# Performance work log

Measured on AMD Instinct MI355X. Metric: run time of the kernel, lower is better.

The kernel has to match this reference:

```python
import jax, jax.numpy as jnp
import numpy as np

N_NODES = 100000

def gcn_conv(x, edge_index, W, b, n_nodes):
    # GCNConv: out = D^{-1/2} (A + I) D^{-1/2} X W + b  (self-loops added)
    src, dst = edge_index[0], edge_index[1]
    loops = jnp.arange(n_nodes, dtype=edge_index.dtype)
    src = jnp.concatenate([src, loops])
    dst = jnp.concatenate([dst, loops])
    deg = jax.ops.segment_sum(jnp.ones_like(dst, dtype=x.dtype), dst, num_segments=n_nodes)
    dinv = jnp.where(deg > 0, jax.lax.rsqrt(deg), 0.0)
    norm = dinv[src] * dinv[dst]  # [E+N]
    h = x @ W  # transform first (small d), then gather/scatter
    msgs = h[src] * norm[:, None]
    out = jax.ops.segment_sum(msgs, dst, num_segments=n_nodes)
    return out + b


def setup_inputs() -> dict:
    key = jax.random.key(0)
    k1, k2, k3, k4, k5, k6 = jax.random.split(key, 6)
    x = jax.random.normal(k1, (N_NODES, 3), dtype=jnp.float32)
    edge_index = jax.random.randint(k2, (2, 2400000), 0, N_NODES, dtype=jnp.int64)
    # Glorot-style init for GCNConv linear weights; zero bias matches PyG default
    W1 = jax.random.normal(k3, (3, 16), dtype=jnp.float32) * (1.0 / np.sqrt(3))
    b1 = jnp.zeros((16,), dtype=jnp.float32)
    W2 = jax.random.normal(k4, (16, 32), dtype=jnp.float32) * (1.0 / np.sqrt(16))
    b2 = jnp.zeros((32,), dtype=jnp.float32)
    return {"x": x, "edge_index": edge_index, "W1": W1, "b1": b1, "W2": W2, "b2": b2}


def reference(x, edge_index, W1, b1, W2, b2):
    n = x.shape[0]
    h = gcn_conv(x, edge_index, W1, b1, n)
    h = jax.nn.relu(h)
    h = gcn_conv(h, edge_index, W2, b2, n)
    # batch is all zeros in the original forward -> single-graph mean pool
    return jnp.mean(h, axis=0, keepdims=True)  # [1, 32]
```

## Files before the change

### kernel.cpp

```cpp
#include <hip/hip_runtime.h>

typedef unsigned int uint;
typedef unsigned long long ull;


#define MAXB  256
#define CAP   16384u
#define BINB  512
#define CHUNK 4096
#define SPL   8
#define PADN  131072
#define AFS   2048.0f
#define AFB   16384
#define AFM   0x1FFFFFu

__device__ __forceinline__ uint slice_lo(uint c, uint s) {
    return (s == 0u) ? 0u : ((c * s / SPL) & ~7u);
}
__device__ __forceinline__ uint slice_hi(uint c, uint s) {
    return (s == SPL - 1u) ? c : ((c * (s + 1u) / SPL) & ~7u);
}

__global__ void __launch_bounds__(BINB)
bin_kernel(const int* __restrict__ key, const int* __restrict__ other,
           uint* __restrict__ cursor, uint* __restrict__ buf, int E) {
    __shared__ uint cnt[MAXB], scanb[MAXB], baseb[MAXB];
    __shared__ uint stage[CHUNK];
    const int tid = threadIdx.x;
    const int e0 = blockIdx.x * CHUNK;
    const int nE = min(CHUNK, E - e0);
    const int my0 = tid * 8;
    const int myc = max(0, min(8, nE - my0));
    if (tid < MAXB) cnt[tid] = 0u;

    uint k8[8], o8[8], r8[8];
    if (myc == 8) {
        int4 ka = ((const int4*)(key + e0))[tid * 2];
        int4 kb = ((const int4*)(key + e0))[tid * 2 + 1];
        int4 oa = ((const int4*)(other + e0))[tid * 2];
        int4 ob = ((const int4*)(other + e0))[tid * 2 + 1];
        k8[0] = ka.x; k8[1] = ka.y; k8[2] = ka.z; k8[3] = ka.w;
        k8[4] = kb.x; k8[5] = kb.y; k8[6] = kb.z; k8[7] = kb.w;
        o8[0] = oa.x; o8[1] = oa.y; o8[2] = oa.z; o8[3] = oa.w;
        o8[4] = ob.x; o8[5] = ob.y; o8[6] = ob.z; o8[7] = ob.w;
    } else {
        for (int r = 0; r < myc; ++r) {
            k8[r] = (uint)key[e0 + my0 + r];
            o8[r] = (uint)other[e0 + my0 + r];
        }
    }
    __syncthreads();
    for (int r = 0; r < myc; ++r) r8[r] = atomicAdd(&cnt[k8[r] >> 9], 1u);
    __syncthreads();
    if (tid < MAXB) scanb[tid] = cnt[tid];
    __syncthreads();
    for (int d = 1; d < MAXB; d <<= 1) {
        uint t = (tid < MAXB && tid >= d) ? scanb[tid - d] : 0u;
        __syncthreads();
        if (tid < MAXB) scanb[tid] += t;
        __syncthreads();
    }
    if (tid < MAXB) baseb[tid] = (uint)tid * CAP + (cnt[tid] ? atomicAdd(&cursor[tid * 16], cnt[tid]) : 0u);
    __syncthreads();
    for (int r = 0; r < myc; ++r) {
        uint b = k8[r] >> 9;
        stage[(scanb[b] - cnt[b]) + r8[r]] = ((k8[r] & 511u) << 17) | o8[r];
    }
    __syncthreads();
    const int wave = tid >> 6, lane = tid & 63;
    for (int b = wave; b < MAXB; b += BINB / 64) {
        uint s0 = scanb[b] - cnt[b], c = cnt[b], gb = baseb[b];
        uint lim = (uint)(b + 1) * CAP;
        for (uint i = lane; i < c; i += 64u) {
            uint gp = gb + i;
            if (gp < lim) buf[gp] = stage[s0 + i];
        }
    }
}

__global__ void __launch_bounds__(256)
deg_kernel(const uint* __restrict__ buf, const uint* __restrict__ curD,
           uint* __restrict__ degg, int n) {
    __shared__ uint dg[512];
    const int tid = threadIdx.x;
    const int b = blockIdx.x >> 3;
    const uint s = blockIdx.x & 7;
    const uint base = (uint)b * CAP;
    const uint c = min(curD[b * 16], CAP);
    const uint lo = slice_lo(c, s), hi = slice_hi(c, s);
    dg[tid] = 0u; dg[tid + 256] = 0u;
    __syncthreads();
    for (uint i0 = lo + (uint)tid * 8u; i0 < hi; i0 += 2048u) {
        uint cnt8 = min(8u, hi - i0);
        uint en[8];
        if (cnt8 == 8u) {
            uint4 a = ((const uint4*)(buf + base + i0))[0];
            uint4 bb = ((const uint4*)(buf + base + i0))[1];
            en[0] = a.x; en[1] = a.y; en[2] = a.z; en[3] = a.w;
            en[4] = bb.x; en[5] = bb.y; en[6] = bb.z; en[7] = bb.w;
        } else {
            for (uint r = 0; r < cnt8; ++r) en[r] = buf[base + i0 + r];
        }
        for (uint r = 0; r < cnt8; ++r) atomicAdd(&dg[en[r] >> 17], 1u);
    }
    __syncthreads();
    for (int t = tid; t < 512; t += 256) {
        int node = (b << 9) + t;
        if (node < n && dg[t]) atomicAdd(&degg[node], dg[t]);
    }
}

__global__ void node1_kernel(const float* __restrict__ x, const uint* __restrict__ degg,
                             float* __restrict__ dinv, float4* __restrict__ xd4, int n) {
    int i = blockIdx.x * blockDim.x + threadIdx.x;
    if (i >= n) return;
    float di = rsqrtf((float)(degg[i] + 1u));
    dinv[i] = di;
    xd4[i] = make_float4(x[3 * i] * di, x[3 * i + 1] * di, x[3 * i + 2] * di, di);
}

__global__ void __launch_bounds__(256)
agg_kernel(const uint* __restrict__ buf, const uint* __restrict__ curD,
           const float4* __restrict__ xd4, ull* __restrict__ accp, int n) {
    __shared__ ull acc[512];
    const int tid = threadIdx.x;
    const int b = blockIdx.x >> 3;
    const uint s = blockIdx.x & 7;
    const uint base = (uint)b * CAP;
    const uint c = min(curD[b * 16], CAP);
    const uint lo = slice_lo(c, s), hi = slice_hi(c, s);
    acc[tid] = 0ull; acc[tid + 256] = 0ull;
    __syncthreads();
    for (uint i0 = lo + (uint)tid * 8u; i0 < hi + 8u * 2048u; i0 += 2048u) {
        if (i0 >= hi) continue;
        uint cnt8 = min(8u, hi - i0);
        uint en[8];
        if (cnt8 == 8u) {
            uint4 a = ((const uint4*)(buf + base + i0))[0];
            uint4 bb = ((const uint4*)(buf + base + i0))[1];
            en[0] = a.x; en[1] = a.y; en[2] = a.z; en[3] = a.w;
            en[4] = bb.x; en[5] = bb.y; en[6] = bb.z; en[7] = bb.w;
        } else {
            for (uint r = 0; r < cnt8; ++r) en[r] = buf[base + i0 + r];
            for (uint r = cnt8; r < 8u; ++r) en[r] = en[0];
        }
        float4 gv[8];
#pragma unroll
        for (int r = 0; r < 8; ++r) gv[r] = xd4[en[r] & 0x1FFFFu];
#pragma unroll
        for (uint r = 0; r < 8u; ++r) {
            if (r < cnt8) {
                uint dl = en[r] >> 17;
                ull f0 = (ull)(uint)((int)rintf(gv[r].x * AFS) + AFB);
                ull f1 = (ull)(uint)((int)rintf(gv[r].y * AFS) + AFB);
                ull f2 = (ull)(uint)((int)rintf(gv[r].z * AFS) + AFB);
                atomicAdd(&acc[dl], f0 | (f1 << 21) | (f2 << 42));
            }
        }
    }
    __syncthreads();
    for (int t = tid; t < 512; t += 256) {
        ull v = acc[t];
        int node = (b << 9) + t;
        if (v && node < n) atomicAdd(&accp[node], v);
    }
}

__global__ void __launch_bounds__(256)
q_kernel(const ull* __restrict__ accp, const uint* __restrict__ degg,
         const float4* __restrict__ xd4, const float* __restrict__ W1,
         const float* __restrict__ b1, uint4* __restrict__ qb,
         float* __restrict__ T, int n) {
    __shared__ float tacc[16];
    const int tid = threadIdx.x;
    if (tid < 16) tacc[tid] = 0.0f;
    __syncthreads();
    int i = blockIdx.x * blockDim.x + tid;
    float sq[16];
    if (i < n) {
        float4 sv = xd4[i];
        float di = sv.w;
        ull v = accp[i];
        int ub = (int)(degg[i] * (uint)AFB);
        const float isc = 1.0f / AFS;
        float a = (float)((int)(uint)(v & AFM) - ub) * isc + sv.x;
        float b = (float)((int)(uint)((v >> 21) & AFM) - ub) * isc + sv.y;
        float c = (float)((int)(uint)((v >> 42) & AFM) - ub) * isc + sv.z;
        float q[16];
#pragma unroll
        for (int k = 0; k < 16; ++k) {
            float h = di * (a * W1[k] + b * W1[16 + k] + c * W1[32 + k]) + b1[k];
            h = fmaxf(h, 0.0f);
            q[k] = di * h;
            sq[k] = di * q[k];
        }
        uint pk[8];
#pragma unroll
        for (int k = 0; k < 8; ++k) {
            uint l = __float_as_uint(q[2 * k]);
            l = (l + 0x7FFFu + ((l >> 16) & 1u)) >> 16;
            uint h2 = __float_as_uint(q[2 * k + 1]);
            h2 = ((h2 + 0x7FFFu + ((h2 >> 16) & 1u)) & 0xFFFF0000u);
            pk[k] = l | h2;
        }
        qb[2 * (size_t)i]     = make_uint4(pk[0], pk[1], pk[2], pk[3]);
        qb[2 * (size_t)i + 1] = make_uint4(pk[4], pk[5], pk[6], pk[7]);
    } else {
#pragma unroll
        for (int k = 0; k < 16; ++k) sq[k] = 0.0f;
    }
#pragma unroll
    for (int k = 0; k < 16; ++k) {
        float v = sq[k];
        for (int off = 32; off > 0; off >>= 1) v += __shfl_down(v, off, 64);
        if ((tid & 63) == 0) atomicAdd(&tacc[k], v);
    }
    __syncthreads();
    if (tid < 16) atomicAdd(&T[tid], tacc[tid]);
}

__global__ void __launch_bounds__(256)
T_kernel(const uint* __restrict__ buf, const uint* __restrict__ curD,
         const float* __restrict__ dinv, const uint4* __restrict__ qb,
         float* __restrict__ T, int n) {
    __shared__ float dt[512];
    __shared__ float tacc[16];
    const int tid = threadIdx.x;
    const int b = blockIdx.x >> 3;
    const uint s = blockIdx.x & 7;
    const uint base = (uint)b * CAP;
    const uint c = min(curD[b * 16], CAP);
    const uint lo = slice_lo(c, s), hi = slice_hi(c, s);
    for (int t = tid; t < 512; t += 256) {
        int node = (b << 9) + t;
        dt[t] = (node < n) ? dinv[node] : 0.0f;
    }
    if (tid < 16) tacc[tid] = 0.0f;
    __syncthreads();
    float rac[16];
#pragma unroll
    for (int k = 0; k < 16; ++k) rac[k] = 0.0f;
    for (uint i0 = lo + (uint)tid * 8u; i0 < hi + 8u * 2048u; i0 += 2048u) {
        if (i0 >= hi) continue;
        uint cnt8 = min(8u, hi - i0);
        uint en[8];
        if (cnt8 == 8u) {
            uint4 a = ((const uint4*)(buf + base + i0))[0];
            uint4 bb = ((const uint4*)(buf + base + i0))[1];
            en[0] = a.x; en[1] = a.y; en[2] = a.z; en[3] = a.w;
            en[4] = bb.x; en[5] = bb.y; en[6] = bb.z; en[7] = bb.w;
        } else {
            for (uint r = 0; r < cnt8; ++r) en[r] = buf[base + i0 + r];
            for (uint r = cnt8; r < 8u; ++r) en[r] = en[0];
        }
        uint4 qa[8], qc[8];
#pragma unroll
        for (int r = 0; r < 8; ++r) {
            uint sv = en[r] & 0x1FFFFu;
            qa[r] = qb[2 * (size_t)sv];
            qc[r] = qb[2 * (size_t)sv + 1];
        }
#pragma unroll
        for (uint r = 0; r < 8u; ++r) {
            if (r < cnt8) {
                float di = dt[en[r] >> 17];
                uint w[8] = {qa[r].x, qa[r].y, qa[r].z, qa[r].w,
                             qc[r].x, qc[r].y, qc[r].z, qc[r].w};
#pragma unroll
                for (int k = 0; k < 8; ++k) {
                    rac[2 * k]     += di * __uint_as_float(w[k] << 16);
                    rac[2 * k + 1] += di * __uint_as_float(w[k] & 0xFFFF0000u);
                }
            }
        }
    }
#pragma unroll
    for (int k = 0; k < 16; ++k) {
        float v = rac[k];
        for (int off = 32; off > 0; off >>= 1) v += __shfl_down(v, off, 64);
        if ((tid & 63) == 0) atomicAdd(&tacc[k], v);
    }
    __syncthreads();
    if (tid < 16) atomicAdd(&T[tid], tacc[tid]);
}

__global__ void out_kernel(const float* __restrict__ T, const float* __restrict__ W2,
                           const float* __restrict__ b2, float* __restrict__ out, float invN) {
    int j = threadIdx.x;
    float s = 0.0f;
#pragma unroll
    for (int k = 0; k < 16; ++k) s += T[k] * W2[k * 32 + j];
    out[j] = b2[j] + invN * s;
}

extern "C" void kernel_launch(void* const* d_in, const int* in_sizes, int n_in,
                              void* d_out, int out_size, void* d_ws, size_t ws_size,
                              hipStream_t stream) {
    const float* x   = (const float*)d_in[0];
    const int*   ei  = (const int*)d_in[1];
    const float* W1  = (const float*)d_in[2];
    const float* b1  = (const float*)d_in[3];
    const float* W2  = (const float*)d_in[4];
    const float* b2  = (const float*)d_in[5];
    float* out = (float*)d_out;

    const int n = in_sizes[0] / 3;
    const int E = in_sizes[1] / 2;
    const int* src = ei;
    const int* dst = ei + E;

    char* p = (char*)d_ws;
    float* T    = (float*)p;    p += 64;
    uint*  curD = (uint*)p;     p += MAXB * 16 * 4;
    uint*  degg = (uint*)p;     p += (size_t)n * 4;
    ull*   accp = (ull*)p;      p += (size_t)n * 8;
    size_t zbytes = (size_t)(p - (char*)d_ws);
    uint*   bufD  = (uint*)p;   p += (size_t)MAXB * CAP * 4;
    float*  dinv  = (float*)p;  p += (size_t)n * 4;
    p = (char*)(((size_t)p + 31) & ~(size_t)31);
    float4* xd4   = (float4*)p; p += (size_t)PADN * 16;
    uint4*  qb    = (uint4*)p;  p += (size_t)PADN * 32;

    const int nb = (n + 511) >> 9;

    hipMemsetAsync(d_ws, 0, zbytes, stream);
    bin_kernel<<<(E + CHUNK - 1) / CHUNK, BINB, 0, stream>>>(dst, src, curD, bufD, E);
    deg_kernel<<<nb * SPL, 256, 0, stream>>>(bufD, curD, degg, n);
    node1_kernel<<<(n + 255) / 256, 256, 0, stream>>>(x, degg, dinv, xd4, n);
    agg_kernel<<<nb * SPL, 256, 0, stream>>>(bufD, curD, xd4, accp, n);
    q_kernel<<<(n + 255) / 256, 256, 0, stream>>>(accp, degg, xd4, W1, b1, qb, T, n);
    T_kernel<<<nb * SPL, 256, 0, stream>>>(bufD, curD, dinv, qb, T, n);
    out_kernel<<<1, 32, 0, stream>>>(T, W2, b2, out, 1.0f / (float)n);
}
```

Baseline: 167.5 us.

## Fuse output GEMV into T_kernel, zero buffers in bin_kernel, coalesce T gathers

The final 32-wide output projection moves into the last-finishing block of T_kernel, found with an atomic ticket counter, which removes one launch. Degree and accumulator zeroing moves from the memset into bin_kernel, so the memset shrinks. The T accumulation switches to fixed-point 64-bit integer atomics so the sum is deterministic regardless of block order. T_kernel's edge loop also changes from 8 contiguous edges per thread to a strided, coalesced 4-edge pattern, trading some load vectorisation for coalesced access.

```diff
diff --git a/kernel.cpp b/kernel.cpp
--- a/kernel.cpp
+++ b/kernel.cpp
@@ -13,6 +13,8 @@
 #define AFS   2048.0f
 #define AFB   16384
 #define AFM   0x1FFFFFu
+#define TFS   1048576.0
+#define TFSI  9.5367431640625e-7
 
 __device__ __forceinline__ uint slice_lo(uint c, uint s) {
     return (s == 0u) ? 0u : ((c * s / SPL) & ~7u);
@@ -23,10 +25,15 @@
 
 __global__ void __launch_bounds__(BINB)
 bin_kernel(const int* __restrict__ key, const int* __restrict__ other,
-           uint* __restrict__ cursor, uint* __restrict__ buf, int E) {
+           uint* __restrict__ cursor, uint* __restrict__ buf,
+           uint* __restrict__ zdeg, ull* __restrict__ zacc, int n, int E) {
     __shared__ uint cnt[MAXB], scanb[MAXB], baseb[MAXB];
     __shared__ uint stage[CHUNK];
     const int tid = threadIdx.x;
+    {
+        int gz = blockIdx.x * BINB + tid;
+        if (gz < n) { zdeg[gz] = 0u; zacc[gz] = 0ull; }
+    }
     const int e0 = blockIdx.x * CHUNK;
     const int nE = min(CHUNK, E - e0);
     const int my0 = tid * 8;
@@ -170,10 +177,10 @@
 q_kernel(const ull* __restrict__ accp, const uint* __restrict__ degg,
          const float4* __restrict__ xd4, const float* __restrict__ W1,
          const float* __restrict__ b1, uint4* __restrict__ qb,
-         float* __restrict__ T, int n) {
-    __shared__ float tacc[16];
-    const int tid = threadIdx.x;
-    if (tid < 16) tacc[tid] = 0.0f;
+         ull* __restrict__ T64, int n) {
+    __shared__ ull tacc64[16];
+    const int tid = threadIdx.x;
+    if (tid < 16) tacc64[tid] = 0ull;
     __syncthreads();
     int i = blockIdx.x * blockDim.x + tid;
     float sq[16];
@@ -213,18 +220,22 @@
     for (int k = 0; k < 16; ++k) {
         float v = sq[k];
         for (int off = 32; off > 0; off >>= 1) v += __shfl_down(v, off, 64);
-        if ((tid & 63) == 0) atomicAdd(&tacc[k], v);
-    }
-    __syncthreads();
-    if (tid < 16) atomicAdd(&T[tid], tacc[tid]);
+        if ((tid & 63) == 0) atomicAdd(&tacc64[k], (ull)(long long)((double)v * TFS + 0.5));
+    }
+    __syncthreads();
+    if (tid < 16) atomicAdd(&T64[tid], tacc64[tid]);
 }
 
 __global__ void __launch_bounds__(256)
 T_kernel(const uint* __restrict__ buf, const uint* __restrict__ curD,
          const float* __restrict__ dinv, const uint4* __restrict__ qb,
-         float* __restrict__ T, int n) {
+         ull* __restrict__ T64, uint* __restrict__ tcount,
+         const float* __restrict__ W2, const float* __restrict__ b2,
+         float* __restrict__ out, int n, int nblk, float invN) {
     __shared__ float dt[512];
-    __shared__ float tacc[16];
+    __shared__ ull tacc64[16];
+    __shared__ float tf[16];
+    __shared__ uint isLast;
     const int tid = threadIdx.x;
     const int b = blockIdx.x >> 3;
     const uint s = blockIdx.x & 7;
@@ -235,34 +246,29 @@
         int node = (b << 9) + t;
         dt[t] = (node < n) ? dinv[node] : 0.0f;
     }
-    if (tid < 16) tacc[tid] = 0.0f;
+    if (tid < 16) tacc64[tid] = 0ull;
     __syncthreads();
     float rac[16];
 #pragma unroll
     for (int k = 0; k < 16; ++k) rac[k] = 0.0f;
-    for (uint i0 = lo + (uint)tid * 8u; i0 < hi + 8u * 2048u; i0 += 2048u) {
-        if (i0 >= hi) continue;
-        uint cnt8 = min(8u, hi - i0);
-        uint en[8];
-        if (cnt8 == 8u) {
-            uint4 a = ((const uint4*)(buf + base + i0))[0];
-            uint4 bb = ((const uint4*)(buf + base + i0))[1];
-            en[0] = a.x; en[1] = a.y; en[2] = a.z; en[3] = a.w;
-            en[4] = bb.x; en[5] = bb.y; en[6] = bb.z; en[7] = bb.w;
-        } else {
-            for (uint r = 0; r < cnt8; ++r) en[r] = buf[base + i0 + r];
-            for (uint r = cnt8; r < 8u; ++r) en[r] = en[0];
-        }
-        uint4 qa[8], qc[8];
-#pragma unroll
-        for (int r = 0; r < 8; ++r) {
+    for (uint g0 = lo; g0 < hi + 1024u * 3u; g0 += 1024u) {
+        if (g0 >= hi) continue;
+        uint en[4]; uint4 qa[4], qc[4];
+#pragma unroll
+        for (int r = 0; r < 4; ++r) {
+            uint i = g0 + (uint)r * 256u + (uint)tid;
+            en[r] = buf[base + (i < hi ? i : lo)];
+        }
+#pragma unroll
+        for (int r = 0; r < 4; ++r) {
             uint sv = en[r] & 0x1FFFFu;
             qa[r] = qb[2 * (size_t)sv];
             qc[r] = qb[2 * (size_t)sv + 1];
         }
 #pragma unroll
-        for (uint r = 0; r < 8u; ++r) {
-            if (r < cnt8) {
+        for (int r = 0; r < 4; ++r) {
+            uint i = g0 + (uint)r * 256u + (uint)tid;
+            if (i < hi) {
                 float di = dt[en[r] >> 17];
                 uint w[8] = {qa[r].x, qa[r].y, qa[r].z, qa[r].w,
                              qc[r].x, qc[r].y, qc[r].z, qc[r].w};
@@ -278,19 +284,29 @@
     for (int k = 0; k < 16; ++k) {
         float v = rac[k];
         for (int off = 32; off > 0; off >>= 1) v += __shfl_down(v, off, 64);
-        if ((tid & 63) == 0) atomicAdd(&tacc[k], v);
-    }
-    __syncthreads();
-    if (tid < 16) atomicAdd(&T[tid], tacc[tid]);
-}
-
-__global__ void out_kernel(const float* __restrict__ T, const float* __restrict__ W2,
-                           const float* __restrict__ b2, float* __restrict__ out, float invN) {
-    int j = threadIdx.x;
-    float s = 0.0f;
-#pragma unroll
-    for (int k = 0; k < 16; ++k) s += T[k] * W2[k * 32 + j];
-    out[j] = b2[j] + invN * s;
+        if ((tid & 63) == 0) atomicAdd(&tacc64[k], (ull)(long long)((double)v * TFS + 0.5));
+    }
+    __syncthreads();
+    if (tid < 16) atomicAdd(&T64[tid], tacc64[tid]);
+    __threadfence();
+    if (tid == 0) {
+        uint prev = atomicAdd(tcount, 1u);
+        isLast = (prev == (uint)(nblk - 1)) ? 1u : 0u;
+    }
+    __syncthreads();
+    if (isLast) {
+        if (tid < 16) {
+            ull tv = atomicAdd(&T64[tid], 0ull);
+            tf[tid] = (float)((double)tv * TFSI);
+        }
+        __syncthreads();
+        if (tid < 32) {
+            float sum = 0.0f;
+#pragma unroll
+            for (int k = 0; k < 16; ++k) sum += tf[k] * W2[k * 32 + tid];
+            out[tid] = b2[tid] + invN * sum;
+        }
+    }
 }
 
 extern "C" void kernel_launch(void* const* d_in, const int* in_sizes, int n_in,
@@ -310,11 +326,12 @@
     const int* dst = ei + E;
 
     char* p = (char*)d_ws;
-    float* T    = (float*)p;    p += 64;
-    uint*  curD = (uint*)p;     p += MAXB * 16 * 4;
-    uint*  degg = (uint*)p;     p += (size_t)n * 4;
-    ull*   accp = (ull*)p;      p += (size_t)n * 8;
+    ull*   T64    = (ull*)p;    p += 128;
+    uint*  tcount = (uint*)p;   p += 64;
+    uint*  curD   = (uint*)p;   p += MAXB * 16 * 4;
     size_t zbytes = (size_t)(p - (char*)d_ws);
+    uint*   degg  = (uint*)p;   p += (size_t)n * 4;
+    ull*    accp  = (ull*)p;    p += (size_t)n * 8;
     uint*   bufD  = (uint*)p;   p += (size_t)MAXB * CAP * 4;
     float*  dinv  = (float*)p;  p += (size_t)n * 4;
     p = (char*)(((size_t)p + 31) & ~(size_t)31);
@@ -322,13 +339,13 @@
     uint4*  qb    = (uint4*)p;  p += (size_t)PADN * 32;
 
     const int nb = (n + 511) >> 9;
+    const int nblkT = nb * SPL;
 
     hipMemsetAsync(d_ws, 0, zbytes, stream);
-    bin_kernel<<<(E + CHUNK - 1) / CHUNK, BINB, 0, stream>>>(dst, src, curD, bufD, E);
+    bin_kernel<<<(E + CHUNK - 1) / CHUNK, BINB, 0, stream>>>(dst, src, curD, bufD, degg, accp, n, E);
     deg_kernel<<<nb * SPL, 256, 0, stream>>>(bufD, curD, degg, n);
     node1_kernel<<<(n + 255) / 256, 256, 0, stream>>>(x, degg, dinv, xd4, n);
     agg_kernel<<<nb * SPL, 256, 0, stream>>>(bufD, curD, xd4, accp, n);
-    q_kernel<<<(n + 255) / 256, 256, 0, stream>>>(accp, degg, xd4, W1, b1, qb, T, n);
-    T_kernel<<<nb * SPL, 256, 0, stream>>>(bufD, curD, dinv, qb, T, n);
-    out_kernel<<<1, 32, 0, stream>>>(T, W2, b2, out, 1.0f / (float)n);
-}
+    q_kernel<<<(n + 255) / 256, 256, 0, stream>>>(accp, degg, xd4, W1, b1, qb, T64, n);
+    T_kernel<<<nblkT, 256, 0, stream>>>(bufD, curD, dinv, qb, T64, tcount, W2, b2, out, n, nblkT, 1.0f / (float)n);
+}
```

Result: slower. 250.8 us (+49.7%).
